# Kernel tuning notes

Measured on AMD Instinct MI355X. Metric: run time of the kernel, lower is better.

Reference implementation:

```python
import jax, jax.numpy as jnp
import numpy as np

D = 1024

def setup_inputs() -> dict:
    key = jax.random.key(0)
    ks = jax.random.split(key, 12)
    B, N, d = 4, 4096, D
    init_std = 0.02 / np.sqrt(d)  # matches _init_weights for value_proj / o_proj
    inp = {
        "h": jax.random.normal(ks[0], (B, N, d), dtype=jnp.float32),
        # relation_encoder: Linear(d, d//2) -> GELU -> Linear(d//2, 1)  (weights stored [in, out])
        "W_re1": jax.random.normal(ks[1], (d, d // 2), dtype=jnp.float32) * 0.02,
        "b_re1": jnp.zeros((d // 2,), dtype=jnp.float32),
        "W_re2": jax.random.normal(ks[2], (d // 2, 1), dtype=jnp.float32) * 0.02,
        "b_re2": jnp.zeros((1,), dtype=jnp.float32),
        # value_proj: Linear(d, d, bias=False), init std = 0.02/sqrt(d)
        "W_v": jax.random.normal(ks[3], (d, d), dtype=jnp.float32) * init_std,
        # relation_transform: Linear(2d, d) -> GELU -> Linear(d, d)
        "W_rt1": jax.random.normal(ks[4], (2 * d, d), dtype=jnp.float32) * 0.02,
        "b_rt1": jnp.zeros((d,), dtype=jnp.float32),
        "W_rt2": jax.random.normal(ks[5], (d, d), dtype=jnp.float32) * 0.02,
        "b_rt2": jnp.zeros((d,), dtype=jnp.float32),
        # o_proj: Linear(d, d, bias=False), init std = 0.02/sqrt(d)
        "W_o": jax.random.normal(ks[6], (d, d), dtype=jnp.float32) * init_std,
    }
    return inp


def reference(h, W_re1, b_re1, W_re2, b_re2, W_v, W_rt1, b_rt1, W_rt2, b_rt2, W_o):
    B, N, d = h.shape
    # relation_encoder MLP -> scalar logit per token (torch GELU is exact erf form)
    hidden = jax.nn.gelu(jnp.einsum('bnd,dk->bnk', h, W_re1) + b_re1, approximate=False)
    relation_logits = (jnp.einsum('bnk,ko->bno', hidden, W_re2) + b_re2)[..., 0]  # [B, N]
    relation_strength = jax.nn.sigmoid(relation_logits)  # [B, N]
    # pointer targets: round(sigmoid * (N-1)) clamped (jnp.round == torch.round, half-to-even)
    relation_targets = jnp.clip(
        jnp.round(relation_strength * (N - 1)).astype(jnp.int32), 0, N - 1
    )  # [B, N]
    # per-token gather of target hidden state within each batch row
    target_features = jnp.take_along_axis(h, relation_targets[..., None], axis=1)  # [B, N, d]
    source_values = jnp.einsum('bnd,de->bne', h, W_v)
    target_values = jnp.einsum('bnd,de->bne', target_features, W_v)
    relation_input = jnp.concatenate([source_values, target_values], axis=-1)  # [B, N, 2d]
    relation_output = jax.nn.gelu(
        jnp.einsum('bnf,fe->bne', relation_input, W_rt1) + b_rt1, approximate=False
    )
    relation_output = jnp.einsum('bne,ef->bnf', relation_output, W_rt2) + b_rt2
    z = jnp.einsum('bnd,de->bne', relation_output, W_o)  # [B, N, d]
    return (z, relation_targets, relation_strength)
```

## Files before the change

kernel.cpp:

```cpp
#include <hip/hip_runtime.h>
#include <math.h>
#include <type_traits>

#define DMODEL 1024
#define NSEQ   4096
#define MTOT   16384

typedef unsigned short ushortT;
typedef __attribute__((ext_vector_type(8))) short short8;
typedef __attribute__((ext_vector_type(4))) float f32x4;

__device__ __forceinline__ float gelu_f(float x) {
    return 0.5f * x * (1.0f + erff(x * 0.70710678118654752440f));
}
__device__ __forceinline__ double gelu_d(double x) {
    return 0.5 * x * (1.0 + erf(x * 0.70710678118654752440));
}
__device__ __forceinline__ ushortT f2bf(float f) {
    unsigned u = __float_as_uint(f);
    u += 0x7FFFu + ((u >> 16) & 1u);
    return (ushortT)(u >> 16);
}
__device__ __forceinline__ float bf2f(ushortT b) {
    return __uint_as_float(((unsigned)b) << 16);
}
__device__ __forceinline__ void gload16(const void* g, void* l) {
    __builtin_amdgcn_global_load_lds(
        (const __attribute__((address_space(1))) unsigned*)g,
        (__attribute__((address_space(3))) unsigned*)l, 16, 0, 0);
}

enum { EPI_BIAS_F32 = 2, EPI_TRANS_BF16 = 3, EPI_PQ = 5 };

template<int EPI, int NXT>
__global__ __launch_bounds__(256)
void mfma_gemm(const ushortT* __restrict__ A, const ushortT* __restrict__ Bt,
               const float* __restrict__ bias, void* __restrict__ Cv,
               void* __restrict__ Cv2, int K, int lda, int ldb, int ldc, int cpx)
{
    __shared__ ushortT As[128 * 32];
    __shared__ ushortT Bs[128 * 32];
    const int tid  = threadIdx.x;
    const int lane = tid & 63;
    const int w    = tid >> 6;
    const int wr   = (w >> 1) * 64;
    const int wc   = (w & 1) * 64;
    const int flat = blockIdx.x + blockIdx.y * NXT;
    const int swz  = (flat & 7) * cpx + (flat >> 3);
    const int n0   = (swz & (NXT - 1)) * 128;
    const int m0   = (swz / NXT) * 128;

    const int lrow = lane >> 2;
    const int lk   = (lane & 3) * 8;

    f32x4 acc[4][4];
    #pragma unroll
    for (int i = 0; i < 4; i++)
        #pragma unroll
        for (int j = 0; j < 4; j++) acc[i][j] = (f32x4){0.f, 0.f, 0.f, 0.f};

    for (int kk = 0; kk < K; kk += 32) {
        #pragma unroll
        for (int i = 0; i < 2; i++) {
            const ushortT* ga = A + (size_t)(m0 + w * 32 + i * 16 + lrow) * lda + kk + lk;
            gload16(ga, &As[(w * 32 + i * 16) * 32]);
            const ushortT* gb = Bt + (size_t)(n0 + w * 32 + i * 16 + lrow) * ldb + kk + lk;
            gload16(gb, &Bs[(w * 32 + i * 16) * 32]);
        }
        __syncthreads();

        const int mi = lane & 15;
        const int ko = (lane >> 4) * 8;
        short8 a[4], b[4];
        #pragma unroll
        for (int i = 0; i < 4; i++)
            a[i] = *(const short8*)&As[(wr + i * 16 + mi) * 32 + ko];
        #pragma unroll
        for (int j = 0; j < 4; j++)
            b[j] = *(const short8*)&Bs[(wc + j * 16 + mi) * 32 + ko];
        #pragma unroll
        for (int i = 0; i < 4; i++)
            #pragma unroll
            for (int j = 0; j < 4; j++)
                acc[i][j] = __builtin_amdgcn_mfma_f32_16x16x32_bf16(a[i], b[j], acc[i][j], 0, 0, 0);
        __syncthreads();
    }

    const int cr = (lane >> 4) * 4;
    const int cc = lane & 15;
    #pragma unroll
    for (int i = 0; i < 4; i++) {
        #pragma unroll
        for (int j = 0; j < 4; j++) {
            const int gr = m0 + wr + i * 16 + cr;
            const int gc = n0 + wc + j * 16 + cc;
            #pragma unroll
            for (int r = 0; r < 4; r++) {
                float v = acc[i][j][r];
                if constexpr (EPI == EPI_BIAS_F32) {
                    ((float*)Cv)[(size_t)(gr + r) * ldc + gc] = v + bias[gc];
                } else if constexpr (EPI == EPI_PQ) {
                    if (gc < 1024)
                        ((float*)Cv)[(size_t)(gr + r) * ldc + gc] = v + bias[gc];
                    else
                        ((ushortT*)Cv2)[(size_t)(gr + r) * ldc + (gc - 1024)] = f2bf(v);
                } else {
                    ((ushortT*)Cv)[(size_t)gc * ldc + (gr + r)] = f2bf(v);
                }
            }
        }
    }
}

__global__ __launch_bounds__(256)
void gelu_gather_k(const float* __restrict__ P, const ushortT* __restrict__ Q,
                   const int* __restrict__ gidx, ushortT* __restrict__ G)
{
    const int m = blockIdx.x;
    int t = gidx[m];
    t = max(0, min(t, MTOT - 1));
    const int c = threadIdx.x * 4;
    float4 p = *(const float4*)(P + (size_t)m * DMODEL + c);
    ushort4 q = *(const ushort4*)(Q + (size_t)t * DMODEL + c);
    ushortT o[4];
    o[0] = f2bf(gelu_f(p.x + bf2f(q.x)));
    o[1] = f2bf(gelu_f(p.y + bf2f(q.y)));
    o[2] = f2bf(gelu_f(p.z + bf2f(q.z)));
    o[3] = f2bf(gelu_f(p.w + bf2f(q.w)));
    *(ulong1*)(G + (size_t)m * DMODEL + c) = *(ulong1*)o;
}

__global__ __launch_bounds__(256)
void wsplit_gemm(const ushortT* __restrict__ Ah, const ushortT* __restrict__ Al,
                 const ushortT* __restrict__ Bh0, const ushortT* __restrict__ Bl0,
                 ushortT* __restrict__ Ct0, int K, int lda, int ldb, int ldc)
{
    __shared__ ushortT Ash[128 * 32], Asl[128 * 32];
    __shared__ ushortT Bsh[128 * 32], Bsl[128 * 32];
    const int tid  = threadIdx.x;
    const int lane = tid & 63;
    const int w    = tid >> 6;
    const int wr   = (w >> 1) * 64;
    const int wc   = (w & 1) * 64;
    const int sel  = blockIdx.y >> 3;
    const int m0   = (blockIdx.y & 7) * 128;
    const int n0   = blockIdx.x * 128;
    const ushortT* Bh = Bh0 + sel * 1024;
    const ushortT* Bl = Bl0 + sel * 1024;
    ushortT* Ct = Ct0 + (size_t)sel * 1024 * 1024;
    const int lrow = lane >> 2;
    const int lk   = (lane & 3) * 8;

    f32x4 acc[4][4];
    #pragma unroll
    for (int i = 0; i < 4; i++)
        #pragma unroll
        for (int j = 0; j < 4; j++) acc[i][j] = (f32x4){0.f, 0.f, 0.f, 0.f};

    for (int kk = 0; kk < K; kk += 32) {
        #pragma unroll
        for (int i = 0; i < 2; i++) {
            const size_t aoff = (size_t)(m0 + w * 32 + i * 16 + lrow) * lda + kk + lk;
            const size_t boff = (size_t)(n0 + w * 32 + i * 16 + lrow) * ldb + kk + lk;
            const int ldst = (w * 32 + i * 16) * 32;
            gload16(Ah + aoff, &Ash[ldst]);
            gload16(Al + aoff, &Asl[ldst]);
            gload16(Bh + boff, &Bsh[ldst]);
            gload16(Bl + boff, &Bsl[ldst]);
        }
        __syncthreads();

        const int mi = lane & 15;
        const int ko = (lane >> 4) * 8;
        short8 ah[4], al[4], bh[4], bl[4];
        #pragma unroll
        for (int i = 0; i < 4; i++) {
            ah[i] = *(const short8*)&Ash[(wr + i * 16 + mi) * 32 + ko];
            al[i] = *(const short8*)&Asl[(wr + i * 16 + mi) * 32 + ko];
        }
        #pragma unroll
        for (int j = 0; j < 4; j++) {
            bh[j] = *(const short8*)&Bsh[(wc + j * 16 + mi) * 32 + ko];
            bl[j] = *(const short8*)&Bsl[(wc + j * 16 + mi) * 32 + ko];
        }
        #pragma unroll
        for (int i = 0; i < 4; i++)
            #pragma unroll
            for (int j = 0; j < 4; j++) {
                acc[i][j] = __builtin_amdgcn_mfma_f32_16x16x32_bf16(ah[i], bh[j], acc[i][j], 0, 0, 0);
                acc[i][j] = __builtin_amdgcn_mfma_f32_16x16x32_bf16(ah[i], bl[j], acc[i][j], 0, 0, 0);
                acc[i][j] = __builtin_amdgcn_mfma_f32_16x16x32_bf16(al[i], bh[j], acc[i][j], 0, 0, 0);
            }
        __syncthreads();
    }

    const int cr = (lane >> 4) * 4;
    const int cc = lane & 15;
    #pragma unroll
    for (int i = 0; i < 4; i++)
        #pragma unroll
        for (int j = 0; j < 4; j++) {
            const int gr = m0 + wr + i * 16 + cr;
            const int gc = n0 + wc + j * 16 + cc;
            #pragma unroll
            for (int r = 0; r < 4; r++)
                Ct[(size_t)gc * ldc + (gr + r)] = f2bf(acc[i][j][r]);
        }
}

__global__ __launch_bounds__(256)
void enc_gemm(const ushortT* __restrict__ Ah, const ushortT* __restrict__ Al,
              const ushortT* __restrict__ Bh, const ushortT* __restrict__ Bl,
              const float* __restrict__ bias, float* __restrict__ C)
{
    __shared__ ushortT Ash[128 * 32], Asl[128 * 32];
    __shared__ ushortT Bsh[128 * 32], Bsl[128 * 32];
    const int tid  = threadIdx.x;
    const int lane = tid & 63;
    const int w    = tid >> 6;
    const int wr   = (w >> 1) * 64;
    const int wc   = (w & 1) * 64;
    const int flat = blockIdx.x + (blockIdx.y << 2);
    const int swz  = (flat & 7) * 64 + (flat >> 3);
    const int n0   = (swz & 3) * 128;
    const int m0   = (swz >> 2) * 128;
    const int lrow = lane >> 2;
    const int lk   = (lane & 3) * 8;

    f32x4 acc[4][4];
    #pragma unroll
    for (int i = 0; i < 4; i++)
        #pragma unroll
        for (int j = 0; j < 4; j++) acc[i][j] = (f32x4){0.f, 0.f, 0.f, 0.f};

    for (int kk = 0; kk < DMODEL; kk += 32) {
        #pragma unroll
        for (int i = 0; i < 2; i++) {
            const size_t aoff = (size_t)(m0 + w * 32 + i * 16 + lrow) * DMODEL + kk + lk;
            const size_t boff = (size_t)(n0 + w * 32 + i * 16 + lrow) * DMODEL + kk + lk;
            const int ldst = (w * 32 + i * 16) * 32;
            gload16(Ah + aoff, &Ash[ldst]);
            gload16(Al + aoff, &Asl[ldst]);
            gload16(Bh + boff, &Bsh[ldst]);
            gload16(Bl + boff, &Bsl[ldst]);
        }
        __syncthreads();

        const int mi = lane & 15;
        const int ko = (lane >> 4) * 8;
        short8 ah[4], al[4], bh[4], bl[4];
        #pragma unroll
        for (int i = 0; i < 4; i++) {
            ah[i] = *(const short8*)&Ash[(wr + i * 16 + mi) * 32 + ko];
            al[i] = *(const short8*)&Asl[(wr + i * 16 + mi) * 32 + ko];
        }
        #pragma unroll
        for (int j = 0; j < 4; j++) {
            bh[j] = *(const short8*)&Bsh[(wc + j * 16 + mi) * 32 + ko];
            bl[j] = *(const short8*)&Bsl[(wc + j * 16 + mi) * 32 + ko];
        }
        #pragma unroll
        for (int i = 0; i < 4; i++)
            #pragma unroll
            for (int j = 0; j < 4; j++) {
                acc[i][j] = __builtin_amdgcn_mfma_f32_16x16x32_bf16(ah[i], bh[j], acc[i][j], 0, 0, 0);
                acc[i][j] = __builtin_amdgcn_mfma_f32_16x16x32_bf16(ah[i], bl[j], acc[i][j], 0, 0, 0);
                acc[i][j] = __builtin_amdgcn_mfma_f32_16x16x32_bf16(al[i], bh[j], acc[i][j], 0, 0, 0);
            }
        __syncthreads();
    }

    const int cr = (lane >> 4) * 4;
    const int cc = lane & 15;
    #pragma unroll
    for (int i = 0; i < 4; i++)
        #pragma unroll
        for (int j = 0; j < 4; j++) {
            const int gr = m0 + wr + i * 16 + cr;
            const int gc = n0 + wc + j * 16 + cc;
            #pragma unroll
            for (int r = 0; r < 4; r++)
                C[(size_t)(gr + r) * 512 + gc] = gelu_f(acc[i][j][r] + bias[gc]);
        }
}

__global__ __launch_bounds__(256)
void target2_k(const float* __restrict__ Genc, const float* __restrict__ W2,
               const float* __restrict__ b2, float* __restrict__ outT,
               float* __restrict__ outS, int* __restrict__ gidx,
               int* __restrict__ cnt, int* __restrict__ list)
{
    const int m = blockIdx.x * 4 + (threadIdx.x >> 6);
    const int lane = threadIdx.x & 63;
    const float* gr = Genc + (size_t)m * 512;
    double s = 0.0;
    #pragma unroll 4
    for (int j = lane; j < 512; j += 64) s = fma((double)gr[j], (double)W2[j], s);
    #pragma unroll
    for (int off = 32; off; off >>= 1) s += __shfl_down(s, off);
    if (lane == 0) {
        double logit = s + (double)b2[0];
        double str = 1.0 / (1.0 + exp(-logit));
        double r = str * (double)(NSEQ - 1);
        double n = rint(r);
        double dist = fabs(r - n);
        n = fmin(fmax(n, 0.0), (double)(NSEQ - 1));
        int t = (int)n;
        outT[m] = (float)t;
        outS[m] = (float)str;
        gidx[m] = ((m >> 12) << 12) + t;
        if (dist > 0.46) {
            int ix = atomicAdd(cnt, 1) & (MTOT - 1);
            list[ix] = m;
        }
    }
}

#define FIX_T 4
__global__ __launch_bounds__(256)
void fixup_k(const float* __restrict__ h, const float* __restrict__ W1,
             const float* __restrict__ b1, const float* __restrict__ W2,
             const float* __restrict__ b2, const int* __restrict__ cnt_p,
             const int* __restrict__ list, float* __restrict__ outT,
             float* __restrict__ outS, int* __restrict__ gidx)
{
    __shared__ float hrow[FIX_T][1024];
    __shared__ double red[4][FIX_T];
    const int tid = threadIdx.x;
    const int cnt = min(*cnt_p, MTOT);
    for (int base = (int)blockIdx.x * FIX_T; base < cnt;
         base += (int)gridDim.x * FIX_T) {
        const int nt = min(FIX_T, cnt - base);
        for (int t = 0; t < nt; t++) {
            const int m = list[base + t];
            const float4* src = (const float4*)(h + (size_t)m * 1024);
            ((float4*)hrow[t])[tid] = src[tid];
        }
        __syncthreads();

        double a[FIX_T][2];
        #pragma unroll
        for (int t = 0; t < FIX_T; t++) { a[t][0] = 0.0; a[t][1] = 0.0; }

        #pragma unroll 4
        for (int k = 0; k < 1024; k++) {
            const double wa = (double)W1[(size_t)k * 512 + tid];
            const double wb = (double)W1[(size_t)k * 512 + tid + 256];
            #pragma unroll
            for (int t = 0; t < FIX_T; t++) {
                const double hv = (double)hrow[t][k];
                a[t][0] = fma(hv, wa, a[t][0]);
                a[t][1] = fma(hv, wb, a[t][1]);
            }
        }

        const double w2a = (double)W2[tid], w2b = (double)W2[tid + 256];
        const double b1a = (double)b1[tid], b1b = (double)b1[tid + 256];
        const int lane = tid & 63, w = tid >> 6;
        #pragma unroll
        for (int t = 0; t < FIX_T; t++) {
            double v = w2a * gelu_d(a[t][0] + b1a) + w2b * gelu_d(a[t][1] + b1b);
            #pragma unroll
            for (int off = 32; off; off >>= 1) v += __shfl_down(v, off);
            if (lane == 0) red[w][t] = v;
        }
        __syncthreads();
        if (tid < nt) {
            const int t = tid;
            double logit = red[0][t] + red[1][t] + red[2][t] + red[3][t] + (double)b2[0];
            double str = 1.0 / (1.0 + exp(-logit));
            double r = str * (double)(NSEQ - 1);
            double n = rint(r);
            n = fmin(fmax(n, 0.0), (double)(NSEQ - 1));
            const int m = list[base + t];
            const int ti = (int)n;
            outT[m] = (float)ti;
            outS[m] = (float)str;
            gidx[m] = ((m >> 12) << 12) + ti;
        }
        __syncthreads();
    }
}

__global__ __launch_bounds__(256)
void biascomb_k(const float* __restrict__ brt2, const float* __restrict__ Wo,
                float* __restrict__ bc)
{
    int j = blockIdx.x * 256 + threadIdx.x;
    float s = 0.f;
    for (int e = 0; e < DMODEL; e++) s = fmaf(brt2[e], Wo[e * DMODEL + j], s);
    bc[j] = s;
}

__global__ __launch_bounds__(256)
void cast_k(const float* __restrict__ x, ushortT* __restrict__ y, int n)
{
    int i = (blockIdx.x * 256 + threadIdx.x) * 4;
    if (i < n) {
        float4 v = *(const float4*)(x + i);
        ushortT o[4] = { f2bf(v.x), f2bf(v.y), f2bf(v.z), f2bf(v.w) };
        *(ulong1*)&y[i] = *(ulong1*)o;
    }
}

__global__ __launch_bounds__(256)
void split_cast_k(const float* __restrict__ x, ushortT* __restrict__ yh,
                  ushortT* __restrict__ yl, int n)
{
    int i = (blockIdx.x * 256 + threadIdx.x) * 4;
    if (i < n) {
        float4 v = *(const float4*)(x + i);
        float vv[4] = { v.x, v.y, v.z, v.w };
        ushortT oh[4], ol[4];
        #pragma unroll
        for (int q = 0; q < 4; q++) {
            oh[q] = f2bf(vv[q]);
            ol[q] = f2bf(vv[q] - bf2f(oh[q]));
        }
        *(ulong1*)&yh[i] = *(ulong1*)oh;
        *(ulong1*)&yl[i] = *(ulong1*)ol;
    }
}

__global__ __launch_bounds__(256)
void transcast_k(const float* __restrict__ W, ushortT* __restrict__ Wt, int K, int N)
{
    __shared__ float t[32][33];
    const int tx = threadIdx.x & 31, ty = threadIdx.x >> 5;
    const int n0 = blockIdx.x * 32, k0 = blockIdx.y * 32;
    #pragma unroll
    for (int r = 0; r < 32; r += 8)
        t[ty + r][tx] = W[(size_t)(k0 + ty + r) * N + n0 + tx];
    __syncthreads();
    #pragma unroll
    for (int r = 0; r < 32; r += 8)
        Wt[(size_t)(n0 + ty + r) * K + k0 + tx] = f2bf(t[tx][ty + r]);
}

__global__ __launch_bounds__(256)
void split_transcast_k(const float* __restrict__ W, ushortT* __restrict__ Wth,
                       ushortT* __restrict__ Wtl, int K, int N)
{
    __shared__ float t[32][33];
    const int tx = threadIdx.x & 31, ty = threadIdx.x >> 5;
    const int n0 = blockIdx.x * 32, k0 = blockIdx.y * 32;
    #pragma unroll
    for (int r = 0; r < 32; r += 8)
        t[ty + r][tx] = W[(size_t)(k0 + ty + r) * N + n0 + tx];
    __syncthreads();
    #pragma unroll
    for (int r = 0; r < 32; r += 8) {
        float x = t[tx][ty + r];
        ushortT hi = f2bf(x);
        Wth[(size_t)(n0 + ty + r) * K + k0 + tx] = hi;
        Wtl[(size_t)(n0 + ty + r) * K + k0 + tx] = f2bf(x - bf2f(hi));
    }
}

extern "C" void kernel_launch(void* const* d_in, const int* in_sizes, int n_in,
                              void* d_out, int out_size, void* d_ws, size_t ws_size,
                              hipStream_t stream)
{
    const float* h     = (const float*)d_in[0];
    const float* W_re1 = (const float*)d_in[1];
    const float* b_re1 = (const float*)d_in[2];
    const float* W_re2 = (const float*)d_in[3];
    const float* b_re2 = (const float*)d_in[4];
    const float* W_v   = (const float*)d_in[5];
    const float* W_rt1 = (const float*)d_in[6];
    const float* b_rt1 = (const float*)d_in[7];
    const float* W_rt2 = (const float*)d_in[8];
    const float* b_rt2 = (const float*)d_in[9];
    const float* W_o   = (const float*)d_in[10];

    float* z    = (float*)d_out;
    float* outT = z + (size_t)MTOT * DMODEL;
    float* outS = outT + MTOT;
    ushortT* Q    = (ushortT*)z;
    ushortT* h_hi = (ushortT*)z + (size_t)MTOT * DMODEL;

    char* ws = (char*)d_ws;
    ushortT* G       = (ushortT*)ws;
    float*   Genc    = (float*)(ws + (32ull  << 20));
    ushortT* h_lo    = (ushortT*)(ws + (64ull  << 20));
    float*   P       = (float*)(ws + (32ull  << 20));
    ushortT* Wrt1t_h = (ushortT*)(ws + (96ull  << 20));
    ushortT* Wrt1t_l = (ushortT*)(ws + (100ull << 20));
    ushortT* Wv_h    = (ushortT*)(ws + (104ull << 20));
    ushortT* Wv_l    = (ushortT*)(ws + (106ull << 20));
    ushortT* Wa_t    = (ushortT*)(ws + (108ull << 20));
    ushortT* Wo_t    = (ushortT*)(ws + (112ull << 20));
    ushortT* Wrt2_b  = (ushortT*)(ws + (114ull << 20));
    ushortT* Wc_t    = (ushortT*)(ws + (116ull << 20));
    ushortT* Wre1t_h = (ushortT*)(ws + (118ull << 20));
    ushortT* Wre1t_l = (ushortT*)(ws + (119ull << 20));
    float*   b_c     = (float*)(ws + (120ull << 20));
    int*     cnt     = (int*)  (ws + (120ull << 20) + 4096);
    int*     gidx    = (int*)  (ws + (120ull << 20) + 8192);
    int*     list    = (int*)  (ws + (120ull << 20) + 8192 + 65536);

    split_cast_k<<<dim3(MTOT * DMODEL / 1024), 256, 0, stream>>>(h, h_hi, h_lo, MTOT * DMODEL);
    split_cast_k<<<dim3(DMODEL * DMODEL / 1024), 256, 0, stream>>>(W_v, Wv_h, Wv_l, DMODEL * DMODEL);
    split_transcast_k<<<dim3(16, 32), 256, 0, stream>>>(W_re1, Wre1t_h, Wre1t_l, DMODEL, 512);
    split_transcast_k<<<dim3(32, 64), 256, 0, stream>>>(W_rt1, Wrt1t_h, Wrt1t_l, 2 * DMODEL, DMODEL);
    cast_k<<<dim3(DMODEL * DMODEL / 1024), 256, 0, stream>>>(W_rt2, Wrt2_b, DMODEL * DMODEL);
    transcast_k<<<dim3(32, 32), 256, 0, stream>>>(W_o, Wo_t, DMODEL, DMODEL);
    biascomb_k<<<dim3(4), 256, 0, stream>>>(b_rt2, W_o, b_c);

    wsplit_gemm<<<dim3(8, 16), 256, 0, stream>>>(Wv_h, Wv_l, Wrt1t_h, Wrt1t_l,
                                                 Wa_t, DMODEL, DMODEL, 2 * DMODEL, DMODEL);

    enc_gemm<<<dim3(4, 128), 256, 0, stream>>>(h_hi, h_lo, Wre1t_h, Wre1t_l, b_re1, Genc);

    hipMemsetAsync(cnt, 0, 4, stream);
    target2_k<<<dim3(MTOT / 4), 256, 0, stream>>>(Genc, W_re2, b_re2, outT, outS, gidx, cnt, list);
    fixup_k<<<dim3(4096), 256, 0, stream>>>(h, W_re1, b_re1, W_re2, b_re2, cnt, list,
                                            outT, outS, gidx);

    mfma_gemm<EPI_TRANS_BF16, 8><<<dim3(8, 8), 256, 0, stream>>>(
        Wrt2_b, Wo_t, nullptr, (void*)Wc_t, nullptr, DMODEL, DMODEL, DMODEL, DMODEL, 8);

    mfma_gemm<EPI_PQ, 16><<<dim3(16, 128), 256, 0, stream>>>(
        h_hi, Wa_t, b_rt1, (void*)P, (void*)Q, DMODEL, DMODEL, DMODEL, DMODEL, 256);

    gelu_gather_k<<<dim3(MTOT), 256, 0, stream>>>(P, Q, gidx, G);

    mfma_gemm<EPI_BIAS_F32, 8><<<dim3(8, 128), 256, 0, stream>>>(
        G, Wc_t, b_c, (void*)z, nullptr, DMODEL, DMODEL, DMODEL, DMODEL, 128);
}
```

Before: 645.0 us.

## Add double-buffered 256x256 pipelined GEMM for the two large projections

Adds a new 512-thread GEMM kernel with 256x256 output tiles, K-step 64 and double-buffered LDS staging. Loads of the next K tile are interleaved with MFMA phases and paced by explicit vmcnt waits, barriers and s_setprio. The two large GEMMs (the h->P/Q projection and the final G->z projection) are switched to it to raise data reuse per tile and hide global-load latency. The trade-off is 128 KB of LDS and 128 accumulators per thread, which cuts occupancy, and there is no LDS swizzle, so bank conflicts are possible.

New measurement: 626.7 us. 2.8% less time.

```diff
diff --git a/kernel.cpp b/kernel.cpp
--- a/kernel.cpp
+++ b/kernel.cpp
@@ -31,6 +31,125 @@
 }
 
 enum { EPI_BIAS_F32 = 2, EPI_TRANS_BF16 = 3, EPI_PQ = 5 };
+
+template<int EPI, int NXT>
+__global__ __launch_bounds__(512, 2)
+void pipe_gemm(const ushortT* __restrict__ A, const ushortT* __restrict__ Bt,
+               const float* __restrict__ bias, void* __restrict__ Cv,
+               void* __restrict__ Cv2, int K, int lda, int ldb, int ldc, int cpx)
+{
+    __shared__ ushortT smem[4 * 16384];
+    const int tid  = threadIdx.x;
+    const int lane = tid & 63;
+    const int w    = tid >> 6;
+    const int wr   = w >> 2;
+    const int wc   = w & 3;
+    const int flat = blockIdx.x + blockIdx.y * NXT;
+    const int swz  = (flat & 7) * cpx + (flat >> 3);
+    const int n0   = (swz & (NXT - 1)) * 256;
+    const int m0   = (swz / NXT) * 256;
+
+    const int srow = tid >> 3;
+    const int scol = (tid & 7) * 8;
+
+#define STG_A(buf, q, k0) gload16(A  + (size_t)(m0 + (q)*64 + srow) * lda + (k0) + scol, \
+                                  (char*)smem + (buf)*32768 + (q)*8192 + w*1024)
+#define STG_B(buf, q, k0) gload16(Bt + (size_t)(n0 + (q)*64 + srow) * ldb + (k0) + scol, \
+                                  (char*)smem + 65536 + (buf)*32768 + (q)*8192 + w*1024)
+#define BAR() asm volatile("s_barrier" ::: "memory")
+
+    f32x4 acc[8][4];
+    #pragma unroll
+    for (int i = 0; i < 8; i++)
+        #pragma unroll
+        for (int j = 0; j < 4; j++) acc[i][j] = (f32x4){0.f, 0.f, 0.f, 0.f};
+
+    const int NT = K >> 6;
+
+    #pragma unroll
+    for (int q = 0; q < 4; q++) { STG_A(0, q, 0); STG_B(0, q, 0); }
+
+    const int mi = lane & 15;
+    const int k8 = (lane >> 4) * 8;
+
+    for (int t = 0; t < NT; ++t) {
+        const int c  = t & 1;
+        const int nb = c ^ 1;
+        const int kn = (t + 1) << 6;
+        const bool hn = (t + 1 < NT);
+
+        if (hn) {
+            STG_A(nb, 0, kn); STG_A(nb, 1, kn);
+            asm volatile("s_waitcnt vmcnt(2)" ::: "memory");
+        } else {
+            asm volatile("s_waitcnt vmcnt(0)" ::: "memory");
+        }
+        BAR();
+
+        short8 bf[4][2];
+        #pragma unroll
+        for (int nf = 0; nf < 4; nf++)
+            #pragma unroll
+            for (int ks = 0; ks < 2; ks++)
+                bf[nf][ks] = *(const short8*)&smem[32768 + c * 16384 +
+                                (wc * 64 + nf * 16 + mi) * 64 + ks * 32 + k8];
+
+        #pragma unroll
+        for (int p = 0; p < 4; p++) {
+            if (p > 0) {
+                if (hn) {
+                    if (p == 1) { STG_A(nb, 2, kn); STG_A(nb, 3, kn); }
+                    if (p == 2) { STG_B(nb, 0, kn); STG_B(nb, 1, kn); }
+                    if (p == 3) { STG_B(nb, 2, kn); STG_B(nb, 3, kn); }
+                }
+                BAR();
+            }
+            short8 af[2][2];
+            #pragma unroll
+            for (int ii = 0; ii < 2; ii++)
+                #pragma unroll
+                for (int ks = 0; ks < 2; ks++)
+                    af[ii][ks] = *(const short8*)&smem[c * 16384 +
+                                    (wr * 128 + (p * 2 + ii) * 16 + mi) * 64 + ks * 32 + k8];
+            __builtin_amdgcn_s_setprio(1);
+            #pragma unroll
+            for (int ks = 0; ks < 2; ks++)
+                #pragma unroll
+                for (int ii = 0; ii < 2; ii++)
+                    #pragma unroll
+                    for (int nf = 0; nf < 4; nf++)
+                        acc[p * 2 + ii][nf] = __builtin_amdgcn_mfma_f32_16x16x32_bf16(
+                            af[ii][ks], bf[nf][ks], acc[p * 2 + ii][nf], 0, 0, 0);
+            __builtin_amdgcn_s_setprio(0);
+        }
+        BAR();
+    }
+
+    const int cr = (lane >> 4) * 4;
+    #pragma unroll
+    for (int i = 0; i < 8; i++) {
+        #pragma unroll
+        for (int j = 0; j < 4; j++) {
+            const int gr = m0 + wr * 128 + i * 16 + cr;
+            const int gc = n0 + wc * 64 + j * 16 + mi;
+            #pragma unroll
+            for (int r = 0; r < 4; r++) {
+                float v = acc[i][j][r];
+                if constexpr (EPI == EPI_BIAS_F32) {
+                    ((float*)Cv)[(size_t)(gr + r) * ldc + gc] = v + bias[gc];
+                } else {
+                    if (gc < 1024)
+                        ((float*)Cv)[(size_t)(gr + r) * ldc + gc] = v + bias[gc];
+                    else
+                        ((ushortT*)Cv2)[(size_t)(gr + r) * ldc + (gc - 1024)] = f2bf(v);
+                }
+            }
+        }
+    }
+#undef STG_A
+#undef STG_B
+#undef BAR
+}
 
 template<int EPI, int NXT>
 __global__ __launch_bounds__(256)
@@ -97,16 +216,10 @@
             #pragma unroll
             for (int r = 0; r < 4; r++) {
                 float v = acc[i][j][r];
-                if constexpr (EPI == EPI_BIAS_F32) {
+                if constexpr (EPI == EPI_BIAS_F32)
                     ((float*)Cv)[(size_t)(gr + r) * ldc + gc] = v + bias[gc];
-                } else if constexpr (EPI == EPI_PQ) {
-                    if (gc < 1024)
-                        ((float*)Cv)[(size_t)(gr + r) * ldc + gc] = v + bias[gc];
-                    else
-                        ((ushortT*)Cv2)[(size_t)(gr + r) * ldc + (gc - 1024)] = f2bf(v);
-                } else {
+                else
                     ((ushortT*)Cv)[(size_t)gc * ldc + (gr + r)] = f2bf(v);
-                }
             }
         }
     }
@@ -520,11 +633,11 @@
     mfma_gemm<EPI_TRANS_BF16, 8><<<dim3(8, 8), 256, 0, stream>>>(
         Wrt2_b, Wo_t, nullptr, (void*)Wc_t, nullptr, DMODEL, DMODEL, DMODEL, DMODEL, 8);
 
-    mfma_gemm<EPI_PQ, 16><<<dim3(16, 128), 256, 0, stream>>>(
-        h_hi, Wa_t, b_rt1, (void*)P, (void*)Q, DMODEL, DMODEL, DMODEL, DMODEL, 256);
+    pipe_gemm<EPI_PQ, 8><<<dim3(8, 64), 512, 0, stream>>>(
+        h_hi, Wa_t, b_rt1, (void*)P, (void*)Q, DMODEL, DMODEL, DMODEL, DMODEL, 64);
 
     gelu_gather_k<<<dim3(MTOT), 256, 0, stream>>>(P, Q, gidx, G);
 
-    mfma_gemm<EPI_BIAS_F32, 8><<<dim3(8, 128), 256, 0, stream>>>(
-        G, Wc_t, b_c, (void*)z, nullptr, DMODEL, DMODEL, DMODEL, DMODEL, 128);
-}
+    pipe_gemm<EPI_BIAS_F32, 4><<<dim3(4, 64), 512, 0, stream>>>(
+        G, Wc_t, b_c, (void*)z, nullptr, DMODEL, DMODEL, DMODEL, DMODEL, 32);
+}
```
